# Optimization experiments

Measured on AMD Instinct MI355X. Metric: run time of the kernel, lower is better.

The kernel has to match this reference:

```python
import jax, jax.numpy as jnp
import numpy as np

S = 50.0
M = 0.5
EPS = 1e-7
NORM_EPS = 1e-12

B, D = 1024, 512
C, K = 50000, 3


def _l2_normalize(x, axis=-1):
    n = jnp.linalg.norm(x, axis=axis, keepdims=True)
    return x / jnp.maximum(n, NORM_EPS)


def setup_inputs() -> dict:
    key = jax.random.key(0)
    k1, k2, k3 = jax.random.split(key, 3)
    embeddings = jax.random.normal(k1, (B, D), dtype=jnp.float32)
    labels = jax.random.randint(k2, (B,), 0, C, dtype=jnp.int64)
    # xavier_uniform over flattened (C*K, D) view
    limit = float(np.sqrt(6.0 / (C * K + D)))
    weight = jax.random.uniform(k3, (C, K, D), dtype=jnp.float32, minval=-limit, maxval=limit)
    return {"embeddings": embeddings, "labels": labels, "weight": weight}


def reference(embeddings, labels, weight):
    ne = _l2_normalize(embeddings, axis=-1)            # [B, D]
    nw = _l2_normalize(weight, axis=-1)                # [C, K, D] (row-wise over D)
    # cosine similarity expressed as a GEMM, then max over subcenters
    cosine = jnp.einsum('bd,ckd->bck', ne, nw)          # [B, C, K]
    cosine_max = jnp.max(cosine, axis=2)                # [B, C]
    theta = jnp.arccos(jnp.clip(cosine_max, -1.0 + EPS, 1.0 - EPS))
    target_logits = jnp.cos(theta + M)                  # [B, C]
    one_hot = jax.nn.one_hot(labels, C, dtype=cosine_max.dtype)
    return S * (one_hot * target_logits + (1.0 - one_hot) * cosine_max)
```

## Files before the change

kernel.cpp:

```cpp
#include <hip/hip_runtime.h>
#include <stdint.h>

#define B_N   1024
#define D_N   512
#define C_N   50000
#define K_N   3
#define CPAD  50048
#define NROWS (CPAD * 4)

#define S_SCALE 50.0f
#define COS_M   0.8775825619f
#define SIN_M   0.4794255386f
#define EPS_C   1e-7f

typedef __bf16 bf16_t;
typedef bf16_t bf16x8 __attribute__((ext_vector_type(8)));
typedef float  f32x4  __attribute__((ext_vector_type(4)));

__device__ __forceinline__ float wave_reduce_sum(float v) {
#pragma unroll
    for (int m = 1; m < 64; m <<= 1) v += __shfl_xor(v, m, 64);
    return v;
}

__device__ __forceinline__ void async_copy16(const void* g, void* l) {
    __builtin_amdgcn_global_load_lds(
        (const __attribute__((address_space(1))) void*)g,
        (__attribute__((address_space(3))) void*)l,
        16, 0, 0);
}

__global__ void k_norm_emb(const float* __restrict__ x, bf16_t* __restrict__ y) {
    const int row  = blockIdx.x * 4 + (threadIdx.x >> 6);
    const int lane = threadIdx.x & 63;
    const float4* p = (const float4*)(x + (size_t)row * D_N + lane * 8);
    float4 a = p[0], b = p[1];
    float s = a.x*a.x + a.y*a.y + a.z*a.z + a.w*a.w
            + b.x*b.x + b.y*b.y + b.z*b.z + b.w*b.w;
    s = wave_reduce_sum(s);
    float sc = 1.0f / fmaxf(sqrtf(s), 1e-12f);
    bf16x8 o;
    o[0] = (bf16_t)(a.x * sc); o[1] = (bf16_t)(a.y * sc);
    o[2] = (bf16_t)(a.z * sc); o[3] = (bf16_t)(a.w * sc);
    o[4] = (bf16_t)(b.x * sc); o[5] = (bf16_t)(b.y * sc);
    o[6] = (bf16_t)(b.z * sc); o[7] = (bf16_t)(b.w * sc);
    *(bf16x8*)(y + (size_t)row * D_N + lane * 8) = o;
}

__global__ void k_norm_w(const float* __restrict__ x, bf16_t* __restrict__ y) {
    const int w    = threadIdx.x >> 6;
    const int lane = threadIdx.x & 63;
    const int base = blockIdx.x * 16 + w * 4;
#pragma unroll
    for (int i = 0; i < 4; ++i) {
        const int row = base + i;
        const float4* p = (const float4*)(x + (size_t)row * D_N + lane * 8);
        float4 a = p[0], b = p[1];
        float s = a.x*a.x + a.y*a.y + a.z*a.z + a.w*a.w
                + b.x*b.x + b.y*b.y + b.z*b.z + b.w*b.w;
        s = wave_reduce_sum(s);
        float sc = 1.0f / fmaxf(sqrtf(s), 1e-12f);
        const size_t orow = (size_t)row + (size_t)(row / 3);
        bf16x8 o;
        o[0] = (bf16_t)(a.x * sc); o[1] = (bf16_t)(a.y * sc);
        o[2] = (bf16_t)(a.z * sc); o[3] = (bf16_t)(a.w * sc);
        o[4] = (bf16_t)(b.x * sc); o[5] = (bf16_t)(b.y * sc);
        o[6] = (bf16_t)(b.z * sc); o[7] = (bf16_t)(b.w * sc);
        *(bf16x8*)(y + orow * D_N + lane * 8) = o;
    }
}

__global__ __launch_bounds__(512, 2) void k_gemm8(const bf16_t* __restrict__ Wn,
                                                  const bf16_t* __restrict__ En,
                                                  const int*    __restrict__ labels,
                                                  float*        __restrict__ out) {
    __shared__ __align__(16) char smem[131072];

    const int tid  = threadIdx.x;
    const int w    = tid >> 6;
    const int lane = tid & 63;
    const int wm   = w >> 2;
    const int wn   = w & 3;
    const int cl   = lane & 15;
    const int quad = lane >> 4;

    const int lid   = blockIdx.x;
    const int nid   = (lid & 7) * 391 + (lid >> 3);
    const int btile = nid & 3;
    const int wtile = nid >> 2;
    const int b0    = btile * 256;
    const size_t r0 = (size_t)wtile * 256;

    const int   srcswz = (((lane & 7) ^ (lane >> 3)) << 4);
    const int   srow   = w * 8 + (lane >> 3);
    const char* Wb = (const char*)Wn;
    const char* Eb = (const char*)En;

    auto stageA = [&](int tile, int h) {
        char* l = smem + (tile & 1) * 65536 + h * 16384 + w * 1024;
        const char* g = Wb + ((r0 + (size_t)(h * 128 + srow)) << 10) + tile * 128 + srcswz;
        async_copy16(g, l);
        async_copy16(g + (64 << 10), l + 8192);
    };
    auto stageB = [&](int tile, int h) {
        char* l = smem + (tile & 1) * 65536 + 32768 + h * 16384 + w * 1024;
        const char* g = Eb + ((size_t)(b0 + h * 128 + srow) << 10) + tile * 128 + srcswz;
        async_copy16(g, l);
        async_copy16(g + (64 << 10), l + 8192);
    };

    const int off0 = cl * 128 + ((      quad * 16) ^ ((lane & 7) << 4));
    const int off1 = cl * 128 + ((64 +  quad * 16) ^ ((lane & 7) << 4));

    f32x4  acc[8][4] = {};
    bf16x8 a[4][2], b[4][2];

    stageB(0, 0); stageB(0, 1); stageA(0, 0); stageA(0, 1);
    asm volatile("s_waitcnt vmcnt(4)" ::: "memory");
    stageB(1, 0); stageB(1, 1); stageA(1, 0);
    asm volatile("s_waitcnt vmcnt(6)" ::: "memory");
    __builtin_amdgcn_s_barrier();

#define MFMA_QUAD(MB, NB)                                                        \
    _Pragma("unroll")                                                            \
    for (int mf = 0; mf < 4; ++mf) {                                             \
        _Pragma("unroll")                                                        \
        for (int nf = 0; nf < 2; ++nf) {                                         \
            acc[(MB)*4+mf][(NB)*2+nf] = __builtin_amdgcn_mfma_f32_16x16x32_bf16( \
                a[mf][0], b[(NB)*2+nf][0], acc[(MB)*4+mf][(NB)*2+nf], 0, 0, 0);  \
            acc[(MB)*4+mf][(NB)*2+nf] = __builtin_amdgcn_mfma_f32_16x16x32_bf16( \
                a[mf][1], b[(NB)*2+nf][1], acc[(MB)*4+mf][(NB)*2+nf], 0, 0, 0);  \
        }                                                                        \
    }

#pragma unroll 2
    for (int t = 0; t < 8; ++t) {
        const char* Ab = smem + (t & 1) * 65536 + wm * 16384;
        const char* Bb = smem + (t & 1) * 65536 + 32768 + (wn >> 1) * 16384 + (wn & 1) * 8192;

#pragma unroll
        for (int mf = 0; mf < 4; ++mf) {
            a[mf][0] = *(const bf16x8*)(Ab + mf * 2048 + off0);
            a[mf][1] = *(const bf16x8*)(Ab + mf * 2048 + off1);
        }
#pragma unroll
        for (int nf = 0; nf < 4; ++nf) {
            b[nf][0] = *(const bf16x8*)(Bb + nf * 2048 + off0);
            b[nf][1] = *(const bf16x8*)(Bb + nf * 2048 + off1);
        }
        if (t < 7) stageA(t + 1, 1);
        __builtin_amdgcn_s_barrier();
        __builtin_amdgcn_s_setprio(1);
        MFMA_QUAD(0, 0)
        __builtin_amdgcn_s_setprio(0);
        __builtin_amdgcn_s_barrier();

        if (t < 6) stageB(t + 2, 0);
        __builtin_amdgcn_s_barrier();
        __builtin_amdgcn_s_setprio(1);
        MFMA_QUAD(0, 1)
        __builtin_amdgcn_s_setprio(0);
        __builtin_amdgcn_s_barrier();

#pragma unroll
        for (int mf = 0; mf < 4; ++mf) {
            a[mf][0] = *(const bf16x8*)(Ab + 8192 + mf * 2048 + off0);
            a[mf][1] = *(const bf16x8*)(Ab + 8192 + mf * 2048 + off1);
        }
        if (t < 6) stageB(t + 2, 1);
        __builtin_amdgcn_s_barrier();
        __builtin_amdgcn_s_setprio(1);
        MFMA_QUAD(1, 1)
        __builtin_amdgcn_s_setprio(0);
        __builtin_amdgcn_s_barrier();

        if (t < 6) stageA(t + 2, 0);
        __builtin_amdgcn_s_barrier();
        __builtin_amdgcn_s_setprio(1);
        MFMA_QUAD(1, 0)
        __builtin_amdgcn_s_setprio(0);
        if (t < 6)       { asm volatile("s_waitcnt vmcnt(6)" ::: "memory"); }
        else if (t == 6) { asm volatile("s_waitcnt vmcnt(0)" ::: "memory"); }
        __builtin_amdgcn_s_barrier();
    }
#undef MFMA_QUAD

    float* So = (float*)smem;
    int lab[4];
#pragma unroll
    for (int n = 0; n < 4; ++n) lab[n] = labels[b0 + wn * 64 + n * 16 + cl];

    const int cb = wtile * 64;
#pragma unroll
    for (int m = 0; m < 8; ++m) {
        const int cls_l = wm * 32 + (m >> 2) * 16 + (m & 3) * 4 + quad;
        const int c = cb + cls_l;
#pragma unroll
        for (int n = 0; n < 4; ++n) {
            float v = fmaxf(fmaxf(acc[m][n][0], acc[m][n][1]), acc[m][n][2]);
            if (c == lab[n]) {
                float x = fminf(fmaxf(v, -1.0f + EPS_C), 1.0f - EPS_C);
                v = x * COS_M - sqrtf(fmaxf(1.0f - x * x, 0.0f)) * SIN_M;
            }
            So[(wn * 64 + n * 16 + cl) * 65 + cls_l] = S_SCALE * v;
        }
    }
    __syncthreads();

    const int row  = tid >> 1;
    const int half = tid & 1;
    float*       gp = out + (size_t)(b0 + row) * C_N + cb + half * 32;
    const float* sp = So + row * 65 + half * 32;
#pragma unroll
    for (int q = 0; q < 8; ++q) {
        const int c = cb + half * 32 + q * 4;
        if (c < C_N) {
            float4 o = make_float4(sp[q*4+0], sp[q*4+1], sp[q*4+2], sp[q*4+3]);
            *(float4*)(gp + q * 4) = o;
        }
    }
}

__global__ void k_fb_norms(const float* __restrict__ emb, const float* __restrict__ w,
                           float* __restrict__ einv, float* __restrict__ winv) {
    const int row  = blockIdx.x * 4 + (threadIdx.x >> 6);
    const int lane = threadIdx.x & 63;
    if (row >= B_N + C_N * K_N) return;
    const float* src = (row < B_N) ? (emb + (size_t)row * D_N)
                                   : (w + (size_t)(row - B_N) * D_N);
    const float4* p = (const float4*)(src + lane * 8);
    float4 a = p[0], b = p[1];
    float s = a.x*a.x + a.y*a.y + a.z*a.z + a.w*a.w
            + b.x*b.x + b.y*b.y + b.z*b.z + b.w*b.w;
    s = wave_reduce_sum(s);
    if (lane == 0) {
        float sc = 1.0f / fmaxf(sqrtf(s), 1e-12f);
        if (row < B_N) einv[row] = sc; else winv[row - B_N] = sc;
    }
}

__global__ void k_fb_gemm(const float* __restrict__ emb, const float* __restrict__ w,
                          const int* __restrict__ labels, const float* __restrict__ einv,
                          const float* __restrict__ winv, float* __restrict__ out) {
    const int b = blockIdx.x;
    const int c = blockIdx.y * 256 + threadIdx.x;
    if (c >= C_N) return;
    const float4* e4 = (const float4*)(emb + (size_t)b * D_N);
    const float es = einv[b];
    float best = -1e30f;
    for (int k = 0; k < K_N; ++k) {
        const float4* w4 = (const float4*)(w + ((size_t)c * K_N + k) * D_N);
        float dot = 0.0f;
#pragma unroll 4
        for (int d = 0; d < D_N / 4; ++d) {
            float4 a = e4[d], bb = w4[d];
            dot += a.x*bb.x + a.y*bb.y + a.z*bb.z + a.w*bb.w;
        }
        dot *= es * winv[c * K_N + k];
        best = fmaxf(best, dot);
    }
    if (c == labels[b]) {
        float x = fminf(fmaxf(best, -1.0f + EPS_C), 1.0f - EPS_C);
        best = x * COS_M - sqrtf(fmaxf(1.0f - x * x, 0.0f)) * SIN_M;
    }
    out[(size_t)b * C_N + c] = S_SCALE * best;
}

extern "C" void kernel_launch(void* const* d_in, const int* in_sizes, int n_in,
                              void* d_out, int out_size, void* d_ws, size_t ws_size,
                              hipStream_t stream) {
    const float* emb    = (const float*)d_in[0];
    const int*   labels = (const int*)d_in[1];
    const float* weight = (const float*)d_in[2];
    float*       out    = (float*)d_out;

    const size_t offW = (size_t)1 << 20;
    const size_t need = offW + (size_t)NROWS * D_N * 2;
    if (ws_size >= need) {
        bf16_t* En = (bf16_t*)d_ws;
        bf16_t* Wn = (bf16_t*)((char*)d_ws + offW);
        k_norm_emb<<<B_N / 4, 256, 0, stream>>>(emb, En);
        k_norm_w<<<(C_N * K_N) / 16, 256, 0, stream>>>(weight, Wn);
        k_gemm8<<<dim3(3128), 512, 0, stream>>>(Wn, En, labels, out);
    } else {
        float* einv = (float*)d_ws;
        float* winv = einv + B_N;
        k_fb_norms<<<(B_N + C_N * K_N) / 4, 256, 0, stream>>>(emb, weight, einv, winv);
        k_fb_gemm<<<dim3(B_N, (C_N + 255) / 256), 256, 0, stream>>>(emb, weight, labels,
                                                                    einv, winv, out);
    }
}
```

Baseline: 719.8 us.

## Switch GEMM to 32x32x16 MFMA tiles with a two-phase load schedule

Replaces the 16x16x32 bf16 MFMA inner loop with 32x32x16 MFMAs, so each wave holds 4x2 32x32 accumulator tiles. The per-iteration schedule drops from four barrier-separated MFMA phases to two, with the A and B tile prefetches issued as pairs. The larger instruction shape is meant to cut LDS fragment reads per flop and reduce barrier count. The epilogue is rewritten for the 32x32 accumulator layout, which risks misindexing and changes register pressure.

```diff
diff --git a/kernel.cpp b/kernel.cpp
--- a/kernel.cpp
+++ b/kernel.cpp
@@ -16,6 +16,7 @@
 typedef __bf16 bf16_t;
 typedef bf16_t bf16x8 __attribute__((ext_vector_type(8)));
 typedef float  f32x4  __attribute__((ext_vector_type(4)));
+typedef float  f32x16 __attribute__((ext_vector_type(16)));
 
 __device__ __forceinline__ float wave_reduce_sum(float v) {
 #pragma unroll
@@ -70,7 +71,7 @@
     }
 }
 
-__global__ __launch_bounds__(512, 2) void k_gemm8(const bf16_t* __restrict__ Wn,
+__global__ __launch_bounds__(512, 2) void k_gemm2(const bf16_t* __restrict__ Wn,
                                                   const bf16_t* __restrict__ En,
                                                   const int*    __restrict__ labels,
                                                   float*        __restrict__ out) {
@@ -81,8 +82,8 @@
     const int lane = tid & 63;
     const int wm   = w >> 2;
     const int wn   = w & 3;
-    const int cl   = lane & 15;
-    const int quad = lane >> 4;
+    const int l5   = lane & 31;
+    const int hi   = lane >> 5;
 
     const int lid   = blockIdx.x;
     const int nid   = (lid & 7) * 391 + (lid >> 3);
@@ -109,102 +110,96 @@
         async_copy16(g + (64 << 10), l + 8192);
     };
 
-    const int off0 = cl * 128 + ((      quad * 16) ^ ((lane & 7) << 4));
-    const int off1 = cl * 128 + ((64 +  quad * 16) ^ ((lane & 7) << 4));
-
-    f32x4  acc[8][4] = {};
-    bf16x8 a[4][2], b[4][2];
-
-    stageB(0, 0); stageB(0, 1); stageA(0, 0); stageA(0, 1);
+    const int sw = (lane & 7) << 4;
+    int colk[4];
+#pragma unroll
+    for (int ks = 0; ks < 4; ++ks) colk[ks] = (ks * 32 + hi * 16) ^ sw;
+    const int aoff = (wm * 128 + l5) * 128;
+    const int boff = 32768 + (wn * 64 + l5) * 128;
+
+    f32x16 acc[4][2] = {};
+    bf16x8 a[2][4], b[2][4];
+
+    stageA(0, 0); stageA(0, 1);
+    stageB(0, 0); stageB(0, 1);
+    stageB(1, 0); stageB(1, 1);
     asm volatile("s_waitcnt vmcnt(4)" ::: "memory");
-    stageB(1, 0); stageB(1, 1); stageA(1, 0);
-    asm volatile("s_waitcnt vmcnt(6)" ::: "memory");
     __builtin_amdgcn_s_barrier();
-
-#define MFMA_QUAD(MB, NB)                                                        \
-    _Pragma("unroll")                                                            \
-    for (int mf = 0; mf < 4; ++mf) {                                             \
-        _Pragma("unroll")                                                        \
-        for (int nf = 0; nf < 2; ++nf) {                                         \
-            acc[(MB)*4+mf][(NB)*2+nf] = __builtin_amdgcn_mfma_f32_16x16x32_bf16( \
-                a[mf][0], b[(NB)*2+nf][0], acc[(MB)*4+mf][(NB)*2+nf], 0, 0, 0);  \
-            acc[(MB)*4+mf][(NB)*2+nf] = __builtin_amdgcn_mfma_f32_16x16x32_bf16( \
-                a[mf][1], b[(NB)*2+nf][1], acc[(MB)*4+mf][(NB)*2+nf], 0, 0, 0);  \
-        }                                                                        \
-    }
 
 #pragma unroll 2
     for (int t = 0; t < 8; ++t) {
-        const char* Ab = smem + (t & 1) * 65536 + wm * 16384;
-        const char* Bb = smem + (t & 1) * 65536 + 32768 + (wn >> 1) * 16384 + (wn & 1) * 8192;
-
-#pragma unroll
-        for (int mf = 0; mf < 4; ++mf) {
-            a[mf][0] = *(const bf16x8*)(Ab + mf * 2048 + off0);
-            a[mf][1] = *(const bf16x8*)(Ab + mf * 2048 + off1);
+        const char* base = smem + (t & 1) * 65536;
+
+#pragma unroll
+        for (int mt = 0; mt < 2; ++mt)
+#pragma unroll
+            for (int ks = 0; ks < 4; ++ks)
+                a[mt][ks] = *(const bf16x8*)(base + aoff + mt * 4096 + colk[ks]);
+#pragma unroll
+        for (int nt = 0; nt < 2; ++nt)
+#pragma unroll
+            for (int ks = 0; ks < 4; ++ks)
+                b[nt][ks] = *(const bf16x8*)(base + boff + nt * 4096 + colk[ks]);
+        if (t < 7) { stageA(t + 1, 0); stageA(t + 1, 1); }
+        __builtin_amdgcn_s_barrier();
+        __builtin_amdgcn_s_setprio(1);
+#pragma unroll
+        for (int ks = 0; ks < 4; ++ks)
+#pragma unroll
+            for (int mt = 0; mt < 2; ++mt)
+#pragma unroll
+                for (int nt = 0; nt < 2; ++nt)
+                    acc[mt][nt] = __builtin_amdgcn_mfma_f32_32x32x16_bf16(
+                        a[mt][ks], b[nt][ks], acc[mt][nt], 0, 0, 0);
+        __builtin_amdgcn_s_setprio(0);
+        __builtin_amdgcn_s_barrier();
+
+#pragma unroll
+        for (int mt = 0; mt < 2; ++mt)
+#pragma unroll
+            for (int ks = 0; ks < 4; ++ks)
+                a[mt][ks] = *(const bf16x8*)(base + aoff + (mt + 2) * 4096 + colk[ks]);
+        if (t < 6) { stageB(t + 2, 0); stageB(t + 2, 1); }
+        __builtin_amdgcn_s_barrier();
+        __builtin_amdgcn_s_setprio(1);
+#pragma unroll
+        for (int ks = 0; ks < 4; ++ks)
+#pragma unroll
+            for (int mt = 0; mt < 2; ++mt)
+#pragma unroll
+                for (int nt = 0; nt < 2; ++nt)
+                    acc[mt + 2][nt] = __builtin_amdgcn_mfma_f32_32x32x16_bf16(
+                        a[mt][ks], b[nt][ks], acc[mt + 2][nt], 0, 0, 0);
+        __builtin_amdgcn_s_setprio(0);
+        if (t < 6)       { asm volatile("s_waitcnt vmcnt(4)" ::: "memory"); }
+        else if (t == 6) { asm volatile("s_waitcnt vmcnt(0)" ::: "memory"); }
+        __builtin_amdgcn_s_barrier();
+    }
+
+    float* So = (float*)smem;
+    int lab[2];
+#pragma unroll
+    for (int nt = 0; nt < 2; ++nt) lab[nt] = labels[b0 + wn * 64 + nt * 32 + l5];
+
+    const int cb = wtile * 64;
+#pragma unroll
+    for (int mt = 0; mt < 4; ++mt)
+#pragma unroll
+        for (int nt = 0; nt < 2; ++nt) {
+            const int batch_local = wn * 64 + nt * 32 + l5;
+#pragma unroll
+            for (int g = 0; g < 4; ++g) {
+                float v = fmaxf(fmaxf(acc[mt][nt][4 * g], acc[mt][nt][4 * g + 1]),
+                                acc[mt][nt][4 * g + 2]);
+                const int cls_l = wm * 32 + mt * 8 + 2 * g + hi;
+                const int c     = cb + cls_l;
+                if (c == lab[nt]) {
+                    float x = fminf(fmaxf(v, -1.0f + EPS_C), 1.0f - EPS_C);
+                    v = x * COS_M - sqrtf(fmaxf(1.0f - x * x, 0.0f)) * SIN_M;
+                }
+                So[batch_local * 65 + cls_l] = S_SCALE * v;
+            }
         }
-#pragma unroll
-        for (int nf = 0; nf < 4; ++nf) {
-            b[nf][0] = *(const bf16x8*)(Bb + nf * 2048 + off0);
-            b[nf][1] = *(const bf16x8*)(Bb + nf * 2048 + off1);
-        }
-        if (t < 7) stageA(t + 1, 1);
-        __builtin_amdgcn_s_barrier();
-        __builtin_amdgcn_s_setprio(1);
-        MFMA_QUAD(0, 0)
-        __builtin_amdgcn_s_setprio(0);
-        __builtin_amdgcn_s_barrier();
-
-        if (t < 6) stageB(t + 2, 0);
-        __builtin_amdgcn_s_barrier();
-        __builtin_amdgcn_s_setprio(1);
-        MFMA_QUAD(0, 1)
-        __builtin_amdgcn_s_setprio(0);
-        __builtin_amdgcn_s_barrier();
-
-#pragma unroll
-        for (int mf = 0; mf < 4; ++mf) {
-            a[mf][0] = *(const bf16x8*)(Ab + 8192 + mf * 2048 + off0);
-            a[mf][1] = *(const bf16x8*)(Ab + 8192 + mf * 2048 + off1);
-        }
-        if (t < 6) stageB(t + 2, 1);
-        __builtin_amdgcn_s_barrier();
-        __builtin_amdgcn_s_setprio(1);
-        MFMA_QUAD(1, 1)
-        __builtin_amdgcn_s_setprio(0);
-        __builtin_amdgcn_s_barrier();
-
-        if (t < 6) stageA(t + 2, 0);
-        __builtin_amdgcn_s_barrier();
-        __builtin_amdgcn_s_setprio(1);
-        MFMA_QUAD(1, 0)
-        __builtin_amdgcn_s_setprio(0);
-        if (t < 6)       { asm volatile("s_waitcnt vmcnt(6)" ::: "memory"); }
-        else if (t == 6) { asm volatile("s_waitcnt vmcnt(0)" ::: "memory"); }
-        __builtin_amdgcn_s_barrier();
-    }
-#undef MFMA_QUAD
-
-    float* So = (float*)smem;
-    int lab[4];
-#pragma unroll
-    for (int n = 0; n < 4; ++n) lab[n] = labels[b0 + wn * 64 + n * 16 + cl];
-
-    const int cb = wtile * 64;
-#pragma unroll
-    for (int m = 0; m < 8; ++m) {
-        const int cls_l = wm * 32 + (m >> 2) * 16 + (m & 3) * 4 + quad;
-        const int c = cb + cls_l;
-#pragma unroll
-        for (int n = 0; n < 4; ++n) {
-            float v = fmaxf(fmaxf(acc[m][n][0], acc[m][n][1]), acc[m][n][2]);
-            if (c == lab[n]) {
-                float x = fminf(fmaxf(v, -1.0f + EPS_C), 1.0f - EPS_C);
-                v = x * COS_M - sqrtf(fmaxf(1.0f - x * x, 0.0f)) * SIN_M;
-            }
-            So[(wn * 64 + n * 16 + cl) * 65 + cls_l] = S_SCALE * v;
-        }
-    }
     __syncthreads();
 
     const int row  = tid >> 1;
@@ -281,7 +276,7 @@
         bf16_t* Wn = (bf16_t*)((char*)d_ws + offW);
         k_norm_emb<<<B_N / 4, 256, 0, stream>>>(emb, En);
         k_norm_w<<<(C_N * K_N) / 16, 256, 0, stream>>>(weight, Wn);
-        k_gemm8<<<dim3(3128), 512, 0, stream>>>(Wn, En, labels, out);
+        k_gemm2<<<dim3(3128), 512, 0, stream>>>(Wn, En, labels, out);
     } else {
         float* einv = (float*)d_ws;
         float* winv = einv + B_N;
```

After: 750.2 us. 1.04x slower.
